# Optimization experiments

Measured on AMD Instinct MI355X. Metric: run time of the kernel, lower is better.

Reference implementation:

```python
import jax, jax.numpy as jnp
import numpy as np

N, D, S, H, QP, VP = 512, 256, 32, 4, 8, 8
PAIR_C = S + 3 * VP          # 56
P3 = H * QP * 3              # 96
FD = P3 + 16                 # 112 (rel + dist rbf)


def _layer_norm(x, scale, offset, eps=1e-5):
    mu = x.mean(-1, keepdims=True)
    var = ((x - mu) ** 2).mean(-1, keepdims=True)
    return (x - mu) * jax.lax.rsqrt(var + eps) * scale + offset


def _distance_rbf(d, bins=16, min_d=0.0, max_d=22.0):
    # Gaussian RBF featurization of pairwise distances (salad distance_rbf).
    step = (max_d - min_d) / bins
    centers = min_d + step * jnp.arange(bins, dtype=d.dtype) + step / 2
    return jnp.exp(-(((d[..., None] - centers) / step) ** 2))


def setup_inputs() -> dict:
    key = jax.random.key(0)
    ks = jax.random.split(key, 16)
    f32 = jnp.float32
    nrm = lambda k, shape, s=1.0: (s * jax.random.normal(k, shape)).astype(f32)
    HS = H * S
    return {
        "local": nrm(ks[0], (N, D)),
        "pos": nrm(ks[1], (N, 5, 3)),
        "resi": jnp.arange(N, dtype=jnp.int32),
        "chain": jax.random.randint(ks[2], (N,), 0, 2, dtype=jnp.int32),
        "batch": jnp.zeros((N,), dtype=jnp.int32),
        "mask": jnp.ones((N,), dtype=bool),
        "q_ln_scale": jnp.ones((S,), f32),
        "q_ln_offset": jnp.zeros((S,), f32),
        "k_ln_scale": jnp.ones((S,), f32),
        "k_ln_offset": jnp.zeros((S,), f32),
        "w_q": nrm(ks[3], (D, HS), D ** -0.5),
        "b_q": jnp.zeros((HS,), f32),
        "w_k": nrm(ks[4], (D, HS), D ** -0.5),
        "b_k": jnp.zeros((HS,), f32),
        "w_v": nrm(ks[5], (D, HS), D ** -0.5),
        "b_v": jnp.zeros((HS,), f32),
        "w_qp": nrm(ks[6], (D, H * QP * 3), 0.1 * D ** -0.5),
        "b_qp": jnp.zeros((H * QP * 3,), f32),
        "w_kp": nrm(ks[7], (D, H * QP * 3), 0.1 * D ** -0.5),
        "b_kp": jnp.zeros((H * QP * 3,), f32),
        "w_vp": nrm(ks[8], (D, H * VP * 3), 0.1 * D ** -0.5),
        "b_vp": jnp.zeros((H * VP * 3,), f32),
        "resi_embedding": nrm(ks[9], (66, PAIR_C), 66 ** -0.5),
        "w_pair": nrm(ks[10], (FD, PAIR_C), FD ** -0.5),
        "w_bias": nrm(ks[11], (FD, H), FD ** -0.5),
        "b_bias": jnp.zeros((H,), f32),
        "gamma": jnp.full((H,), np.log(np.e - 1.0), f32),
        "w_out": nrm(ks[12], (H * PAIR_C, D), (H * PAIR_C) ** -0.5),
    }


def reference(local, pos, resi, chain, batch, mask,
              q_ln_scale, q_ln_offset, k_ln_scale, k_ln_offset,
              w_q, b_q, w_k, b_k, w_v, b_v,
              w_qp, b_qp, w_kp, b_kp, w_vp, b_vp,
              resi_embedding, w_pair, w_bias, b_bias, gamma, w_out):
    n = local.shape[0]
    ca = pos[:, 1]  # [n,3]

    q = _layer_norm((local @ w_q + b_q).reshape(n, H, S), q_ln_scale, q_ln_offset)
    k = _layer_norm((local @ w_k + b_k).reshape(n, H, S), k_ln_scale, k_ln_offset)
    v = (local @ w_v + b_v).reshape(n, H, S)
    qp = (local @ w_qp + b_qp).reshape(n, H, QP, 3) + ca[:, None, None]
    kp = (local @ w_kp + b_kp).reshape(n, H, QP, 3) + ca[:, None, None]
    vp = (local @ w_vp + b_vp).reshape(n, H, VP, 3) + ca[:, None, None]
    value = jnp.concatenate((v, vp.reshape(n, H, 3 * VP)), axis=-1)  # [n,H,56]

    same_batch = batch[:, None] == batch[None, :]
    pair_mask = (mask[:, None] & mask[None, :]) & same_batch  # [n,n]

    inner = jnp.einsum('ihc,jhc->ijh', q * jnp.sqrt(1.0 / S), k)  # [n,n,H]
    diff = qp[:, None] - kp[None, :]                 # [n,n,H,QP,3]
    point_att = -(diff ** 2).sum(axis=(-1, -2))      # [n,n,H]
    rel = diff.reshape(n, n, P3)                     # [n,n,96]

    dca = 10.0 * ca
    dist = jnp.sqrt(((dca[:, None] - dca[None, :]) ** 2).sum(-1) + 1e-6)
    dist = _distance_rbf(dist)                       # [n,n,16]

    resi_dist = jnp.clip(resi[:, None] - resi[None, :], -32, 32)
    other_chain = chain[:, None] != chain[None, :]
    rdist = jnp.where(other_chain, 65, resi_dist + 32)
    emb = resi_embedding[rdist]                      # [n,n,56]

    feat = jnp.concatenate((rel, dist), axis=-1)     # [n,n,112]
    pair = emb + feat @ w_pair                       # [n,n,56]
    bias = feat @ w_bias + b_bias                    # [n,n,H]
    pair = pair[:, :, None, :] + value[None]         # [n,n,H,56]

    w_C = jnp.sqrt(2.0 / (9 * QP))
    point_scale = jax.nn.softplus(gamma).reshape(1, 1, H) * w_C / 2

    attn = (inner + point_scale * point_att + bias) * jnp.sqrt(1.0 / 3.0)
    attn = jnp.where(pair_mask[..., None], attn, -1e9)
    attn = jax.nn.softmax(attn, axis=1)
    attn = jnp.where(pair_mask[..., None], attn, 0.0)

    result = jnp.einsum('ijh,ijhc->ihc', attn, pair).reshape(n, -1)  # [n,224]
    return result @ w_out                             # [n,D]
```

## Files before the change

kernel.cpp:

```cpp
#include <hip/hip_runtime.h>
#include <hip/hip_bf16.h>
#include <cstddef>

#define N_NODES 512
#define DIM     256
#define H_HEADS 4
#define PAIR_CN 56
#define P3_N    96
#define FD_N    112
#define HPC     224

typedef _Float16 h2v  __attribute__((ext_vector_type(2)));
typedef _Float16 f16x8 __attribute__((ext_vector_type(8)));
typedef float    f32x4 __attribute__((ext_vector_type(4)));

__device__ __forceinline__ bool mask_true(const void* m, int idx) {
    if (((const unsigned char*)m)[idx] != 0) return true;
    return ((const int*)m)[idx] != 0;
}
__device__ __forceinline__ unsigned packh2(float a, float b) {
    _Float16 ha = (_Float16)a, hb = (_Float16)b;
    unsigned short ua, ub;
    __builtin_memcpy(&ua, &ha, 2); __builtin_memcpy(&ub, &hb, 2);
    return (unsigned)ua | ((unsigned)ub << 16);
}
__device__ __forceinline__ float h2lof(unsigned u) {
    unsigned short t = (unsigned short)(u & 0xffff);
    _Float16 h; __builtin_memcpy(&h, &t, 2); return (float)h;
}
__device__ __forceinline__ float h2hif(unsigned u) {
    unsigned short t = (unsigned short)(u >> 16);
    _Float16 h; __builtin_memcpy(&h, &t, 2); return (float)h;
}
__device__ __forceinline__ float dot2u(unsigned a, unsigned b, float c) {
#if __has_builtin(__builtin_amdgcn_fdot2)
    h2v ha, hb;
    __builtin_memcpy(&ha, &a, 4);
    __builtin_memcpy(&hb, &b, 4);
    return __builtin_amdgcn_fdot2(ha, hb, c, false);
#else
    return c + h2lof(a)*h2lof(b) + h2hif(a)*h2hif(b);
#endif
}
__device__ __forceinline__ f32x4 mfma16(uint4 a, uint4 b, f32x4 c) {
    f16x8 af, bf;
    __builtin_memcpy(&af, &a, 16);
    __builtin_memcpy(&bf, &b, 16);
    return __builtin_amdgcn_mfma_f32_16x16x32_f16(af, bf, c, 0, 0, 0);
}

__global__ __launch_bounds__(512) void proj_kernel(
    const float* __restrict__ local, const float* __restrict__ pos,
    const float* __restrict__ qls, const float* __restrict__ qlo,
    const float* __restrict__ kls, const float* __restrict__ klo,
    const float* __restrict__ w_q, const float* __restrict__ b_q,
    const float* __restrict__ w_k, const float* __restrict__ b_k,
    const float* __restrict__ w_v, const float* __restrict__ b_v,
    const float* __restrict__ w_qp, const float* __restrict__ b_qp,
    const float* __restrict__ w_kp, const float* __restrict__ b_kp,
    const float* __restrict__ w_vp, const float* __restrict__ b_vp,
    const float* __restrict__ w_bias, const float* __restrict__ b_bias,
    const float* __restrict__ gamma,
    const float* __restrict__ remb, const float* __restrict__ w_pair,
    const float* __restrict__ w_out,
    unsigned* __restrict__ qnP, unsigned* __restrict__ knT4,
    unsigned* __restrict__ qpP, unsigned* __restrict__ kpT4,
    unsigned* __restrict__ BF,
    unsigned* __restrict__ woPk, unsigned* __restrict__ wp2,
    unsigned* __restrict__ remb2,
    float* __restrict__ jinfo, float* __restrict__ iinfo)
{
    const int i0 = blockIdx.x * 2;
    const int tid = threadIdx.x;

    __shared__ float xL[2][DIM];
    __shared__ float qraw[2][128];
    __shared__ float kraw[2][128];
    __shared__ float stat[2][16];
    __shared__ float qpL[2][P3_N];
    __shared__ float kpbL[2][P3_N];
    __shared__ float wbS[384];

    if (blockIdx.x < 16) {
        for (int t = blockIdx.x*512 + tid; t < 33656; t += 8192) {
            if (t < 28672) {
                const int t2 = t >> 8, colx = t & 255;
                woPk[t] = packh2(w_out[(size_t)(2*t2)*DIM + colx],
                                 w_out[(size_t)(2*t2 + 1)*DIM + colx]);
            } else if (t < 31808) {
                const int v = t - 28672, f2 = v / 56, cx = v % 56;
                wp2[v] = packh2(w_pair[(2*f2)*PAIR_CN + cx],
                                w_pair[(2*f2 + 1)*PAIR_CN + cx]);
            } else {
                const int v = t - 31808, r2 = v / 56, cx = v % 56;
                remb2[v] = packh2(remb[(2*r2)*PAIR_CN + cx],
                                  remb[(2*r2 + 1)*PAIR_CN + cx]);
            }
        }
    }

    {
        const int r = tid >> 8, d = tid & 255;
        xL[r][d] = local[(size_t)(i0 + r) * DIM + d];
    }
    if (tid < 384) wbS[tid] = w_bias[tid];
    __syncthreads();

    const int cstBF = ((i0 >> 5) << 8) + (((i0 >> 3) & 3) << 6) + ((i0 >> 1) & 3);

    if (tid < 336) {
        const int colg = tid >> 1, dh = tid & 1;
        const int col = colg * 4;
        const float* w; int width, c, seg;
        if      (col < 128) { w = w_q;  c = col;       width = 128; seg = 0; }
        else if (col < 256) { w = w_k;  c = col - 128; width = 128; seg = 1; }
        else if (col < 384) { w = w_v;  c = col - 256; width = 128; seg = 2; }
        else if (col < 480) { w = w_qp; c = col - 384; width = 96;  seg = 3; }
        else if (col < 576) { w = w_kp; c = col - 480; width = 96;  seg = 4; }
        else                { w = w_vp; c = col - 576; width = 96;  seg = 5; }

        float acc[2][4] = {{0.f,0.f,0.f,0.f},{0.f,0.f,0.f,0.f}};
        const float* wc = w + c;
        const int dbase = dh * 128;
#pragma unroll 1
        for (int bb = 0; bb < 16; ++bb) {
            const int d0 = dbase + bb*8;
            const float4 wv0 = *(const float4*)(wc + (size_t)(d0 + 0)*width);
            const float4 wv1 = *(const float4*)(wc + (size_t)(d0 + 1)*width);
            const float4 wv2 = *(const float4*)(wc + (size_t)(d0 + 2)*width);
            const float4 wv3 = *(const float4*)(wc + (size_t)(d0 + 3)*width);
            const float4 wv4 = *(const float4*)(wc + (size_t)(d0 + 4)*width);
            const float4 wv5 = *(const float4*)(wc + (size_t)(d0 + 5)*width);
            const float4 wv6 = *(const float4*)(wc + (size_t)(d0 + 6)*width);
            const float4 wv7 = *(const float4*)(wc + (size_t)(d0 + 7)*width);
#pragma unroll
            for (int r = 0; r < 2; ++r) {
                const float x0 = xL[r][d0 + 0], x1 = xL[r][d0 + 1];
                const float x2 = xL[r][d0 + 2], x3 = xL[r][d0 + 3];
                const float x4 = xL[r][d0 + 4], x5 = xL[r][d0 + 5];
                const float x6 = xL[r][d0 + 6], x7 = xL[r][d0 + 7];
                acc[r][0] += x0*wv0.x + x1*wv1.x + x2*wv2.x + x3*wv3.x
                           + x4*wv4.x + x5*wv5.x + x6*wv6.x + x7*wv7.x;
                acc[r][1] += x0*wv0.y + x1*wv1.y + x2*wv2.y + x3*wv3.y
                           + x4*wv4.y + x5*wv5.y + x6*wv6.y + x7*wv7.y;
                acc[r][2] += x0*wv0.z + x1*wv1.z + x2*wv2.z + x3*wv3.z
                           + x4*wv4.z + x5*wv5.z + x6*wv6.z + x7*wv7.z;
                acc[r][3] += x0*wv0.w + x1*wv1.w + x2*wv2.w + x3*wv3.w
                           + x4*wv4.w + x5*wv5.w + x6*wv6.w + x7*wv7.w;
            }
        }
#pragma unroll
        for (int r = 0; r < 2; ++r)
#pragma unroll
            for (int e = 0; e < 4; ++e)
                acc[r][e] += __shfl_xor(acc[r][e], 1);

        if (dh == 0) {
            const float cax0 = pos[i0*15+3],     cay0 = pos[i0*15+4],     caz0 = pos[i0*15+5];
            const float cax1 = pos[(i0+1)*15+3], cay1 = pos[(i0+1)*15+4], caz1 = pos[(i0+1)*15+5];
            float fr0[4], fr1[4];
            const bool isKp = (seg == 4), isQp = (seg == 3);
#pragma unroll
            for (int e = 0; e < 4; ++e) {
                const int cc = c + e;
                const float v0 = acc[0][e], v1 = acc[1][e];
                if (seg == 0) {
                    qraw[0][cc] = v0 + b_q[cc];
                    qraw[1][cc] = v1 + b_q[cc];
                } else if (seg == 1) {
                    kraw[0][cc] = v0 + b_k[cc];
                    kraw[1][cc] = v1 + b_k[cc];
                } else if (seg == 2) {
                    const int h = cc >> 5, sc = cc & 31;
                    const int colF = h*PAIR_CN + sc;
                    BF[(colF >> 4)*4096 + (colF & 15)*4 + cstBF] =
                        packh2(v0 + b_v[cc], v1 + b_v[cc]);
                } else if (seg == 3) {
                    const int x = cc % 3;
                    const float cav0 = (x==0)?cax0:((x==1)?cay0:caz0);
                    const float cav1 = (x==0)?cax1:((x==1)?cay1:caz1);
                    const float r0 = v0 + b_qp[cc] + cav0;
                    const float r1 = v1 + b_qp[cc] + cav1;
                    fr0[e] = r0; fr1[e] = r1;
                    qpL[0][cc] = r0; qpL[1][cc] = r1;
                } else if (seg == 4) {
                    const int x = cc % 3;
                    const float cav0 = (x==0)?cax0:((x==1)?cay0:caz0);
                    const float cav1 = (x==0)?cax1:((x==1)?cay1:caz1);
                    const float r0 = v0 + b_kp[cc] + cav0;
                    const float r1 = v1 + b_kp[cc] + cav1;
                    fr0[e] = r0; fr1[e] = r1;
                    const int colF = 224 + cc;
                    BF[(colF >> 4)*4096 + (colF & 15)*4 + cstBF] = packh2(r0, r1);
                    kpbL[0][cc] = (float)(_Float16)r0;
                    kpbL[1][cc] = (float)(_Float16)r1;
                } else {
                    const int h = cc / 24, rr = cc % 24, x = cc % 3;
                    const float cav0 = (x==0)?cax0:((x==1)?cay0:caz0);
                    const float cav1 = (x==0)?cax1:((x==1)?cay1:caz1);
                    const int colF = h*PAIR_CN + 32 + rr;
                    BF[(colF >> 4)*4096 + (colF & 15)*4 + cstBF] =
                        packh2(v0 + b_vp[cc] + cav0, v1 + b_vp[cc] + cav1);
                }
            }
            if (isQp) {
                const int f2 = c >> 1;
                qpP[(size_t)i0*48 + f2]         = packh2(fr0[0], fr0[1]);
                qpP[(size_t)i0*48 + f2 + 1]     = packh2(fr0[2], fr0[3]);
                qpP[(size_t)(i0+1)*48 + f2]     = packh2(fr1[0], fr1[1]);
                qpP[(size_t)(i0+1)*48 + f2 + 1] = packh2(fr1[2], fr1[3]);
            }
            if (isKp) {
                const int f2 = c >> 1;
                const int fq = f2 >> 2;
                kpT4[((size_t)fq*N_NODES + i0    )*4 + (f2 & 3)]       = packh2(fr0[0], fr0[1]);
                kpT4[((size_t)fq*N_NODES + i0    )*4 + ((f2 + 1) & 3)] = packh2(fr0[2], fr0[3]);
                kpT4[((size_t)fq*N_NODES + i0 + 1)*4 + (f2 & 3)]       = packh2(fr1[0], fr1[1]);
                kpT4[((size_t)fq*N_NODES + i0 + 1)*4 + ((f2 + 1) & 3)] = packh2(fr1[2], fr1[3]);
            }
        }
    }
    __syncthreads();

    if (tid < 16) {
        const int r = tid >> 3, t = tid & 7;
        const float* src = (t < 4) ? qraw[r] : kraw[r];
        const int h = t & 3, base = (t < 4) ? 0 : 8;
        float mu = 0.f;
        for (int c = 0; c < 32; ++c) mu += src[h*32 + c];
        mu *= (1.f/32.f);
        float var = 0.f;
        for (int c = 0; c < 32; ++c) { float d = src[h*32 + c] - mu; var += d*d; }
        var *= (1.f/32.f);
        stat[r][base + h*2 + 0] = mu;
        stat[r][base + h*2 + 1] = var;
    }
    __syncthreads();

    {
        const int r = tid >> 8, u = tid & 255;
        const int i = i0 + r;
        if (u < 128) {
            const int h = u >> 5, sidx = u & 31;
            const float mu = stat[r][h*2], var = stat[r][h*2+1];
            float v = (qraw[r][u] - mu) * rsqrtf(var + 1e-5f) * qls[sidx] + qlo[sidx];
            v *= 0.17677669529663687f;
            const float vo = __shfl_xor(v, 1);
            if (!(u & 1)) qnP[(size_t)i*64 + (u >> 1)] = packh2(v, vo);
        } else {
            const int u2 = u - 128, h = u2 >> 5, sidx = u2 & 31;
            const float mu = stat[r][8 + h*2], var = stat[r][9 + h*2];
            float v = (kraw[r][u2] - mu) * rsqrtf(var + 1e-5f) * kls[sidx] + klo[sidx];
            const float vo = __shfl_xor(v, 1);
            if (!(u2 & 1))
                knT4[(((size_t)(u2 >> 3))*N_NODES + i)*4 + ((u2 >> 1) & 3)] = packh2(v, vo);
        }
    }

    if (tid < 64) {
        const int r = tid >> 5, h = (tid >> 3) & 3, ks = tid & 7;
        float uacc = 0.f, tacc = 0.f;
#pragma unroll
        for (int f = ks; f < P3_N; f += 8) {
            float wb = wbS[f*4 + h];
            uacc += qpL[r][f] * wb;
            tacc += kpbL[r][f] * wb;
        }
        float nq = 0.f, nk = 0.f;
#pragma unroll
        for (int f = h*24 + ks*3; f < h*24 + ks*3 + 3; ++f) {
            nq += qpL[r][f]*qpL[r][f];
            nk += kpbL[r][f]*kpbL[r][f];
        }
        uacc += __shfl_xor(uacc,1); uacc += __shfl_xor(uacc,2); uacc += __shfl_xor(uacc,4);
        tacc += __shfl_xor(tacc,1); tacc += __shfl_xor(tacc,2); tacc += __shfl_xor(tacc,4);
        nq   += __shfl_xor(nq,1);   nq   += __shfl_xor(nq,2);   nq   += __shfl_xor(nq,4);
        nk   += __shfl_xor(nk,1);   nk   += __shfl_xor(nk,2);   nk   += __shfl_xor(nk,4);
        if (ks == 0) {
            const int n = i0 + r;
            const float ps = log1pf(expf(gamma[h])) * (1.0f/12.0f);
            iinfo[n*4 + h] = -ps*nq + uacc + b_bias[h];
            jinfo[n*8 + h] = -ps*nk - tacc;
            if (h == 0) {
                jinfo[n*8 + 4] = 10.f * pos[n*15 + 3];
                jinfo[n*8 + 5] = 10.f * pos[n*15 + 4];
                jinfo[n*8 + 6] = 10.f * pos[n*15 + 5];
                jinfo[n*8 + 7] = 0.f;
            }
        }
    }
}

__global__ __launch_bounds__(1024, 4) void attn_kernel(
    const unsigned* __restrict__ qnP, const unsigned* __restrict__ knT4,
    const unsigned* __restrict__ qpP, const unsigned* __restrict__ kpT4,
    const unsigned* __restrict__ BF,
    const unsigned* __restrict__ woPk, const unsigned* __restrict__ wp2,
    const unsigned* __restrict__ remb2,
    const float* __restrict__ jinfo, const float* __restrict__ iinfo,
    const int* __restrict__ resi, const int* __restrict__ chain,
    const int* __restrict__ batch, const void* __restrict__ maskp,
    const float* __restrict__ w_bias, const float* __restrict__ gamma,
    float* __restrict__ out)
{
    const int ib   = blockIdx.x * 2;
    const int tid  = threadIdx.x;
    const int lane = tid & 63;
    const int wv   = tid >> 6;
    const int hp   = tid >> 9;
    const int j    = tid & 511;

    __shared__ unsigned qpkL[2][64];
    __shared__ unsigned qspkL[2][48];
    __shared__ unsigned wbPk[H_HEADS][8];
    __shared__ __align__(16) unsigned rbfP[2][N_NODES][9];
    __shared__ __align__(16) unsigned attnH2[8][260];
    __shared__ float    mxW[16][4], smW[16][4];
    __shared__ float    asL2[2][H_HEADS];
    __shared__ float    qpiL2[2][P3_N];
    __shared__ float    GLfF2[2][H_HEADS][P3_N];
    __shared__ float    GLfR2[2][H_HEADS][16];
    __shared__ unsigned GLf22[2][H_HEADS][56];
    __shared__ unsigned abktP2[2][H_HEADS][33];
    __shared__ float    resL2[2][HPC];
    __shared__ unsigned resH2[2][FD_N];
    __shared__ float    abktW8[8][2][H_HEADS][66];

    if (tid < 128) {
        const int r = tid >> 6, u = tid & 63;
        qpkL[r][u] = qnP[(size_t)(ib + r)*64 + u];
    } else if (tid < 224) {
        const int v = tid - 128, r = v / 48, f2 = v % 48;
        const int h = f2 / 12;
        const float ps2 = 2.f * log1pf(expf(gamma[h])) * (1.0f/12.0f);
        const unsigned u = qpP[(size_t)(ib + r)*48 + f2];
        qspkL[r][f2] = packh2(ps2*h2lof(u), ps2*h2hif(u));
    } else if (tid < 320) {
        const int v = tid - 224, r = v / 48, f2 = v % 48;
        const unsigned u = qpP[(size_t)(ib + r)*48 + f2];
        qpiL2[r][2*f2]   = h2lof(u);
        qpiL2[r][2*f2+1] = h2hif(u);
    } else if (tid < 352) {
        const int v = tid - 320, h = v >> 3, e = v & 7;
        wbPk[h][e] = packh2(w_bias[(P3_N + 2*e)*H_HEADS + h],
                            w_bias[(P3_N + 2*e + 1)*H_HEADS + h]);
    }
    for (int t = tid; t < 8*2*H_HEADS*66; t += 1024) ((float*)abktW8)[t] = 0.f;

    const int  ri0 = resi[ib], ri1 = resi[ib+1];
    const int  ch0 = chain[ib], ch1 = chain[ib+1];
    const int  ba0 = batch[ib], ba1 = batch[ib+1];
    const bool mi0 = mask_true(maskp, ib), mi1 = mask_true(maskp, ib+1);
    const float dix0 = jinfo[(size_t)ib*8+4], diy0 = jinfo[(size_t)ib*8+5], diz0 = jinfo[(size_t)ib*8+6];
    const float dix1 = jinfo[(size_t)(ib+1)*8+4], diy1 = jinfo[(size_t)(ib+1)*8+5], diz1 = jinfo[(size_t)(ib+1)*8+6];

    const float inv3  = 0.57735026918962576f;
    const float rstep = 0.72727272727272727f;

    const float4 vq4 = *(const float4*)(jinfo + (size_t)j*8);
    const float4 dj4 = *(const float4*)(jinfo + (size_t)j*8 + 4);
    const float4 ciA = *(const float4*)(iinfo + (size_t)ib*4);
    const float4 ciB = *(const float4*)(iinfo + (size_t)(ib+1)*4);
    const float vqa[4] = {vq4.x, vq4.y, vq4.z, vq4.w};
    const float cia[2][4] = {{ciA.x, ciA.y, ciA.z, ciA.w},
                             {ciB.x, ciB.y, ciB.z, ciB.w}};
    {
        const float dx = (hp ? dix1 : dix0) - dj4.x;
        const float dy = (hp ? diy1 : diy0) - dj4.y;
        const float dz = (hp ? diz1 : diz0) - dj4.z;
        const float dist = sqrtf(dx*dx + dy*dy + dz*dz + 1e-6f);
#pragma unroll
        for (int p = 0; p < 8; ++p) {
            const float u0 = (dist - (1.375f*(float)(2*p)   + 0.6875f)) * rstep;
            const float u1 = (dist - (1.375f*(float)(2*p+1) + 0.6875f)) * rstep;
            rbfP[hp][j][p] = packh2(__expf(-u0*u0), __expf(-u1*u1));
        }
    }
    const int  rj = resi[j], cj = chain[j], bj = batch[j];
    const bool mj = mask_true(maskp, j);
    bool pmv[2];
    int  rdv[2];
    pmv[0] = mi0 && mj && (ba0 == bj);
    pmv[1] = mi1 && mj && (ba1 == bj);
    rdv[0] = (ch0 != cj) ? 65 : (min(max(ri0 - rj, -32), 32) + 32);
    rdv[1] = (ch1 != cj) ? 65 : (min(max(ri1 - rj, -32), 32) + 32);
    __syncthreads();

    float lv[2][2];
    {
        const int h0 = hp*2, h1 = hp*2 + 1;
        const uint4* kcol = (const uint4*)knT4 + j;
        const uint4* pcol = (const uint4*)kpT4 + j;
        const uint4 ka0 = kcol[(size_t)(h0*4 + 0)*N_NODES];
        const uint4 ka1 = kcol[(size_t)(h0*4 + 1)*N_NODES];
        const uint4 ka2 = kcol[(size_t)(h0*4 + 2)*N_NODES];
        const uint4 ka3 = kcol[(size_t)(h0*4 + 3)*N_NODES];
        const uint4 kb0 = kcol[(size_t)(h1*4 + 0)*N_NODES];
        const uint4 kb1 = kcol[(size_t)(h1*4 + 1)*N_NODES];
        const uint4 kb2 = kcol[(size_t)(h1*4 + 2)*N_NODES];
        const uint4 kb3 = kcol[(size_t)(h1*4 + 3)*N_NODES];
        const uint4 pa0 = pcol[(size_t)(h0*3 + 0)*N_NODES];
        const uint4 pa1 = pcol[(size_t)(h0*3 + 1)*N_NODES];
        const uint4 pa2 = pcol[(size_t)(h0*3 + 2)*N_NODES];
        const uint4 pb0 = pcol[(size_t)(h1*3 + 0)*N_NODES];
        const uint4 pb1 = pcol[(size_t)(h1*3 + 1)*N_NODES];
        const uint4 pb2 = pcol[(size_t)(h1*3 + 2)*N_NODES];
        const uint4 rr0a = *(const uint4*)&rbfP[0][j][0];
        const uint4 rr0b = *(const uint4*)&rbfP[0][j][4];
        const uint4 rr1a = *(const uint4*)&rbfP[1][j][0];
        const uint4 rr1b = *(const uint4*)&rbfP[1][j][4];
        const uint4 w0a = *(const uint4*)&wbPk[h0][0];
        const uint4 w0b = *(const uint4*)&wbPk[h0][4];
        const uint4 w1a = *(const uint4*)&wbPk[h1][0];
        const uint4 w1b = *(const uint4*)&wbPk[h1][4];
#pragma unroll
        for (int r = 0; r < 2; ++r) {
            const uint4* qk4 = (const uint4*)&qpkL[r][0];
            const uint4* qs4 = (const uint4*)&qspkL[r][0];
            const uint4 rra = r ? rr1a : rr0a;
            const uint4 rrb = r ? rr1b : rr0b;
            float a0 = 0.f;
            {
                const uint4 q0 = qk4[h0*4 + 0], q1 = qk4[h0*4 + 1];
                const uint4 q2 = qk4[h0*4 + 2], q3 = qk4[h0*4 + 3];
                a0 = dot2u(ka0.x, q0.x, a0); a0 = dot2u(ka0.y, q0.y, a0);
                a0 = dot2u(ka0.z, q0.z, a0); a0 = dot2u(ka0.w, q0.w, a0);
                a0 = dot2u(ka1.x, q1.x, a0); a0 = dot2u(ka1.y, q1.y, a0);
                a0 = dot2u(ka1.z, q1.z, a0); a0 = dot2u(ka1.w, q1.w, a0);
                a0 = dot2u(ka2.x, q2.x, a0); a0 = dot2u(ka2.y, q2.y, a0);
                a0 = dot2u(ka2.z, q2.z, a0); a0 = dot2u(ka2.w, q2.w, a0);
                a0 = dot2u(ka3.x, q3.x, a0); a0 = dot2u(ka3.y, q3.y, a0);
                a0 = dot2u(ka3.z, q3.z, a0); a0 = dot2u(ka3.w, q3.w, a0);
                const uint4 s0 = qs4[h0*3 + 0], s1 = qs4[h0*3 + 1], s2 = qs4[h0*3 + 2];
                a0 = dot2u(pa0.x, s0.x, a0); a0 = dot2u(pa0.y, s0.y, a0);
                a0 = dot2u(pa0.z, s0.z, a0); a0 = dot2u(pa0.w, s0.w, a0);
                a0 = dot2u(pa1.x, s1.x, a0); a0 = dot2u(pa1.y, s1.y, a0);
                a0 = dot2u(pa1.z, s1.z, a0); a0 = dot2u(pa1.w, s1.w, a0);
                a0 = dot2u(pa2.x, s2.x, a0); a0 = dot2u(pa2.y, s2.y, a0);
                a0 = dot2u(pa2.z, s2.z, a0); a0 = dot2u(pa2.w, s2.w, a0);
                a0 = dot2u(rra.x, w0a.x, a0); a0 = dot2u(rra.y, w0a.y, a0);
                a0 = dot2u(rra.z, w0a.z, a0); a0 = dot2u(rra.w, w0a.w, a0);
                a0 = dot2u(rrb.x, w0b.x, a0); a0 = dot2u(rrb.y, w0b.y, a0);
                a0 = dot2u(rrb.z, w0b.z, a0); a0 = dot2u(rrb.w, w0b.w, a0);
            }
            lv[r][0] = pmv[r] ? (a0 + cia[r][h0] + vqa[h0]) * inv3 : -1e9f;
            float a1 = 0.f;
            {
                const uint4 q0 = qk4[h1*4 + 0], q1 = qk4[h1*4 + 1];
                const uint4 q2 = qk4[h1*4 + 2], q3 = qk4[h1*4 + 3];
                a1 = dot2u(kb0.x, q0.x, a1); a1 = dot2u(kb0.y, q0.y, a1);
                a1 = dot2u(kb0.z, q0.z, a1); a1 = dot2u(kb0.w, q0.w, a1);
                a1 = dot2u(kb1.x, q1.x, a1); a1 = dot2u(kb1.y, q1.y, a1);
                a1 = dot2u(kb1.z, q1.z, a1); a1 = dot2u(kb1.w, q1.w, a1);
                a1 = dot2u(kb2.x, q2.x, a1); a1 = dot2u(kb2.y, q2.y, a1);
                a1 = dot2u(kb2.z, q2.z, a1); a1 = dot2u(kb2.w, q2.w, a1);
                a1 = dot2u(kb3.x, q3.x, a1); a1 = dot2u(kb3.y, q3.y, a1);
                a1 = dot2u(kb3.z, q3.z, a1); a1 = dot2u(kb3.w, q3.w, a1);
                const uint4 s0 = qs4[h1*3 + 0], s1 = qs4[h1*3 + 1], s2 = qs4[h1*3 + 2];
                a1 = dot2u(pb0.x, s0.x, a1); a1 = dot2u(pb0.y, s0.y, a1);
                a1 = dot2u(pb0.z, s0.z, a1); a1 = dot2u(pb0.w, s0.w, a1);
                a1 = dot2u(pb1.x, s1.x, a1); a1 = dot2u(pb1.y, s1.y, a1);
                a1 = dot2u(pb1.z, s1.z, a1); a1 = dot2u(pb1.w, s1.w, a1);
                a1 = dot2u(pb2.x, s2.x, a1); a1 = dot2u(pb2.y, s2.y, a1);
                a1 = dot2u(pb2.z, s2.z, a1); a1 = dot2u(pb2.w, s2.w, a1);
                a1 = dot2u(rra.x, w1a.x, a1); a1 = dot2u(rra.y, w1a.y, a1);
                a1 = dot2u(rra.z, w1a.z, a1); a1 = dot2u(rra.w, w1a.w, a1);
                a1 = dot2u(rrb.x, w1b.x, a1); a1 = dot2u(rrb.y, w1b.y, a1);
                a1 = dot2u(rrb.z, w1b.z, a1); a1 = dot2u(rrb.w, w1b.w, a1);
            }
            lv[r][1] = pmv[r] ? (a1 + cia[r][h1] + vqa[h1]) * inv3 : -1e9f;
        }
    }

    {
        float mx[4] = {lv[0][0], lv[0][1], lv[1][0], lv[1][1]};
#pragma unroll
        for (int off = 1; off < 64; off <<= 1) {
#pragma unroll
            for (int s = 0; s < 4; ++s) mx[s] = fmaxf(mx[s], __shfl_xor(mx[s], off));
        }
        if (lane == 0) *(float4*)&mxW[wv][0] = make_float4(mx[0], mx[1], mx[2], mx[3]);
        __syncthreads();
        float mxg[4] = {-1e30f, -1e30f, -1e30f, -1e30f};
        const int wbase = hp*8;
#pragma unroll
        for (int w = 0; w < 8; ++w) {
            const float4 m = *(const float4*)&mxW[wbase + w][0];
            mxg[0] = fmaxf(mxg[0], m.x); mxg[1] = fmaxf(mxg[1], m.y);
            mxg[2] = fmaxf(mxg[2], m.z); mxg[3] = fmaxf(mxg[3], m.w);
        }
        float e[4], sm[4];
        e[0] = pmv[0] ? __expf(lv[0][0] - mxg[0]) : 0.f;
        e[1] = pmv[0] ? __expf(lv[0][1] - mxg[1]) : 0.f;
        e[2] = pmv[1] ? __expf(lv[1][0] - mxg[2]) : 0.f;
        e[3] = pmv[1] ? __expf(lv[1][1] - mxg[3]) : 0.f;
#pragma unroll
        for (int s = 0; s < 4; ++s) sm[s] = e[s];
#pragma unroll
        for (int off = 1; off < 64; off <<= 1) {
#pragma unroll
            for (int s = 0; s < 4; ++s) sm[s] += __shfl_xor(sm[s], off);
        }
        if (lane == 0) *(float4*)&smW[wv][0] = make_float4(sm[0], sm[1], sm[2], sm[3]);
        __syncthreads();
        float smt[4] = {0.f, 0.f, 0.f, 0.f};
#pragma unroll
        for (int w = 0; w < 8; ++w) {
            const float4 m = *(const float4*)&smW[wbase + w][0];
            smt[0] += m.x; smt[1] += m.y; smt[2] += m.z; smt[3] += m.w;
        }
        float p[4];
#pragma unroll
        for (int s = 0; s < 4; ++s) {
            const float rden = 1.f / fmaxf(smt[s], 1e-37f);
            p[s] = e[s] * rden;
        }
        const int h0 = hp*2;
        atomicAdd(&abktW8[wv & 7][0][h0    ][rdv[0]], p[0]);
        atomicAdd(&abktW8[wv & 7][0][h0 + 1][rdv[0]], p[1]);
        atomicAdd(&abktW8[wv & 7][1][h0    ][rdv[1]], p[2]);
        atomicAdd(&abktW8[wv & 7][1][h0 + 1][rdv[1]], p[3]);
        if (j == 0) {
            asL2[0][h0]     = smt[0] / fmaxf(smt[0], 1e-37f);
            asL2[0][h0 + 1] = smt[1] / fmaxf(smt[1], 1e-37f);
            asL2[1][h0]     = smt[2] / fmaxf(smt[2], 1e-37f);
            asL2[1][h0 + 1] = smt[3] / fmaxf(smt[3], 1e-37f);
        }
#pragma unroll
        for (int s = 0; s < 4; ++s) {
            const float po = __shfl_xor(p[s], 1);
            if (!(j & 1)) {
                const int r = s >> 1, hh = s & 1;
                attnH2[r*4 + h0 + hh][j >> 1] = packh2(p[s], po);
            }
        }
    }
    __syncthreads();

    if (wv < 14) {
        const int row = lane & 15;
        const int ntA = wv;
        const int ntB = (wv < 6) ? (wv + 14) : -1;
        f32x4 accA = {0.f,0.f,0.f,0.f};
        f32x4 accB = {0.f,0.f,0.f,0.f};
        const uint4* bfp = (const uint4*)BF;
#pragma unroll 4
        for (int kt = 0; kt < 16; ++kt) {
            uint4 au = make_uint4(0u, 0u, 0u, 0u);
            if (row < 8) au = *(const uint4*)&attnH2[row][kt*16 + (lane >> 4)*4];
            const uint4 bA = bfp[(ntA*16 + kt)*64 + lane];
            accA = mfma16(au, bA, accA);
            if (ntB >= 0) {
                const uint4 bB = bfp[(ntB*16 + kt)*64 + lane];
                accB = mfma16(au, bB, accB);
            }
        }
        if (lane < 32) {
            const int r = lane >> 4, c16 = lane & 15;
            {
                const int s = ntA*16 + c16;
                if (s < HPC) {
                    resL2[r][s] = ((const float*)&accA)[s / PAIR_CN];
                } else {
                    const int f = s - HPC;
                    GLfF2[r][0][f] = accA[0];
                    GLfF2[r][1][f] = accA[1];
                    GLfF2[r][2][f] = accA[2];
                    GLfF2[r][3][f] = accA[3];
                }
            }
            if (ntB >= 0) {
                const int s = ntB*16 + c16;
                if (s < HPC) {
                    resL2[r][s] = ((const float*)&accB)[s / PAIR_CN];
                } else {
                    const int f = s - HPC;
                    GLfF2[r][0][f] = accB[0];
                    GLfF2[r][1][f] = accB[1];
                    GLfF2[r][2][f] = accB[2];
                    GLfF2[r][3][f] = accB[3];
                }
            }
        }
    } else {
        const int r = wv - 14;
        const int b = lane >> 2, q = lane & 3;
        const int w = b >> 1;
        const bool hi = (b & 1);
        float a[4] = {0.f, 0.f, 0.f, 0.f};
#pragma unroll 4
        for (int jpp = q*64; jpp < q*64 + 64; ++jpp) {
            const unsigned r0 = rbfP[r][2*jpp][w];
            const unsigned r1 = rbfP[r][2*jpp + 1][w];
            const unsigned ee = hi ? ((r0 >> 16) | (r1 & 0xffff0000u))
                                   : ((r0 & 0xffffu) | (r1 << 16));
            a[0] = dot2u(ee, attnH2[r*4 + 0][jpp], a[0]);
            a[1] = dot2u(ee, attnH2[r*4 + 1][jpp], a[1]);
            a[2] = dot2u(ee, attnH2[r*4 + 2][jpp], a[2]);
            a[3] = dot2u(ee, attnH2[r*4 + 3][jpp], a[3]);
        }
#pragma unroll
        for (int h = 0; h < 4; ++h) {
            a[h] += __shfl_xor(a[h], 1);
            a[h] += __shfl_xor(a[h], 2);
            if (q == 0) GLfR2[r][h][b] = a[h];
        }
    }
    __syncthreads();

    for (int t = tid; t < 448; t += 1024) {
        const int r = t / 224, v = t % 224, h = v / 56, f2 = v % 56;
        if (f2 < 48) {
            GLf22[r][h][f2] = packh2(qpiL2[r][2*f2]*asL2[r][h]     - GLfF2[r][h][2*f2],
                                     qpiL2[r][2*f2 + 1]*asL2[r][h] - GLfF2[r][h][2*f2 + 1]);
        } else {
            GLf22[r][h][f2] = packh2(GLfR2[r][h][(f2 - 48)*2], GLfR2[r][h][(f2 - 48)*2 + 1]);
        }
    }
    for (int t = tid; t < 264; t += 1024) {
        const int r = t / 132, v = t % 132, h = v / 33, r2 = v % 33;
        float s0 = 0.f, s1 = 0.f;
#pragma unroll
        for (int w = 0; w < 8; ++w) {
            s0 += abktW8[w][r][h][2*r2];
            s1 += abktW8[w][r][h][2*r2 + 1];
        }
        abktP2[r][h][r2] = packh2(s0, s1);
    }
    __syncthreads();

    if (tid < HPC) {
        const int h = tid / PAIR_CN, c = tid - h*PAIR_CN;
        float r0 = resL2[0][tid];
        float r1 = resL2[1][tid];
        {
            unsigned buf[16];
#pragma unroll
            for (int t = 0; t < 16; ++t) buf[t] = remb2[t*56 + c];
#pragma unroll
            for (int t = 0; t < 16; ++t) {
                r0 = dot2u(buf[t], abktP2[0][h][t], r0);
                r1 = dot2u(buf[t], abktP2[1][h][t], r1);
            }
#pragma unroll
            for (int t = 0; t < 16; ++t) buf[t] = remb2[(16 + t)*56 + c];
#pragma unroll
            for (int t = 0; t < 16; ++t) {
                r0 = dot2u(buf[t], abktP2[0][h][16 + t], r0);
                r1 = dot2u(buf[t], abktP2[1][h][16 + t], r1);
            }
            const unsigned b32 = remb2[32*56 + c];
            r0 = dot2u(b32, abktP2[0][h][32], r0);
            r1 = dot2u(b32, abktP2[1][h][32], r1);
        }
        {
            unsigned buf[14];
#pragma unroll
            for (int qq = 0; qq < 4; ++qq) {
#pragma unroll
                for (int t = 0; t < 14; ++t) buf[t] = wp2[(qq*14 + t)*56 + c];
#pragma unroll
                for (int t = 0; t < 14; ++t) {
                    r0 = dot2u(buf[t], GLf22[0][h][qq*14 + t], r0);
                    r1 = dot2u(buf[t], GLf22[1][h][qq*14 + t], r1);
                }
            }
        }
        resL2[0][tid] = r0;
        resL2[1][tid] = r1;
    }
    __syncthreads();

    if (tid < 2*FD_N) {
        const int r = tid / FD_N, t2 = tid % FD_N;
        resH2[r][t2] = packh2(resL2[r][2*t2], resL2[r][2*t2 + 1]);
    }
    __syncthreads();

    if (tid < 512) {
        const int col = tid >> 1, ph = tid & 1;
        float o0 = 0.f, o1 = 0.f;
        unsigned buf[14];
#pragma unroll
        for (int qq = 0; qq < 4; ++qq) {
            const int base = ph*56 + qq*14;
#pragma unroll
            for (int t = 0; t < 14; ++t) buf[t] = woPk[(base + t)*256 + col];
#pragma unroll
            for (int t = 0; t < 14; ++t) {
                o0 = dot2u(buf[t], resH2[0][base + t], o0);
                o1 = dot2u(buf[t], resH2[1][base + t], o1);
            }
        }
        o0 += __shfl_xor(o0, 1);
        o1 += __shfl_xor(o1, 1);
        if (ph == 0) {
            out[(size_t)ib*DIM + col]       = o0;
            out[(size_t)(ib + 1)*DIM + col] = o1;
        }
    }
}

extern "C" void kernel_launch(void* const* d_in, const int* in_sizes, int n_in,
                              void* d_out, int out_size, void* d_ws, size_t ws_size,
                              hipStream_t stream) {
    (void)in_sizes; (void)n_in; (void)out_size; (void)ws_size;
    const float* local = (const float*)d_in[0];
    const float* pos   = (const float*)d_in[1];
    const int*   resi  = (const int*)d_in[2];
    const int*   chain = (const int*)d_in[3];
    const int*   batch = (const int*)d_in[4];
    const void*  maskp = d_in[5];
    const float* qls   = (const float*)d_in[6];
    const float* qlo   = (const float*)d_in[7];
    const float* kls   = (const float*)d_in[8];
    const float* klo   = (const float*)d_in[9];
    const float* w_q   = (const float*)d_in[10];
    const float* b_q   = (const float*)d_in[11];
    const float* w_k   = (const float*)d_in[12];
    const float* b_k   = (const float*)d_in[13];
    const float* w_v   = (const float*)d_in[14];
    const float* b_v   = (const float*)d_in[15];
    const float* w_qp  = (const float*)d_in[16];
    const float* b_qp  = (const float*)d_in[17];
    const float* w_kp  = (const float*)d_in[18];
    const float* b_kp  = (const float*)d_in[19];
    const float* w_vp  = (const float*)d_in[20];
    const float* b_vp  = (const float*)d_in[21];
    const float* remb  = (const float*)d_in[22];
    const float* w_pair= (const float*)d_in[23];
    const float* w_bias= (const float*)d_in[24];
    const float* b_bias= (const float*)d_in[25];
    const float* gamma = (const float*)d_in[26];
    const float* w_out = (const float*)d_in[27];

    char* ws = (char*)d_ws;
    unsigned* qnP   = (unsigned*)(ws);
    unsigned* qpP   = (unsigned*)(ws + 131072);
    unsigned* knT4  = (unsigned*)(ws + 229376);
    unsigned* kpT4  = (unsigned*)(ws + 360448);
    unsigned* BF    = (unsigned*)(ws + 458752);
    float*    jinf  = (float*)(ws + 786432);
    float*    iinf  = (float*)(ws + 802816);
    unsigned* woPk  = (unsigned*)(ws + 811008);
    unsigned* wp2   = (unsigned*)(ws + 925696);
    unsigned* remb2 = (unsigned*)(ws + 938240);

    proj_kernel<<<N_NODES / 2, 512, 0, stream>>>(
        local, pos, qls, qlo, kls, klo,
        w_q, b_q, w_k, b_k, w_v, b_v,
        w_qp, b_qp, w_kp, b_kp, w_vp, b_vp,
        w_bias, b_bias, gamma,
        remb, w_pair, w_out,
        qnP, knT4, qpP, kpT4, BF,
        woPk, wp2, remb2, jinf, iinf);

    attn_kernel<<<N_NODES / 2, 1024, 0, stream>>>(
        qnP, knT4, qpP, kpT4, BF,
        woPk, wp2, remb2, jinf, iinf,
        resi, chain, batch, maskp,
        w_bias, gamma,
        (float*)d_out);
}
```

Measured before the change: 53.62 us.

## Fuse projection and attention kernels with a software grid barrier

Merges the projection kernel and the attention kernel into one persistent launch of 1024-thread blocks. A global atomic-counter barrier, reset with a memset before each launch, separates the two phases. The projection reduction over the feature dimension is split four ways instead of two, with an extra shuffle to combine the partial sums. The aim is to remove the second kernel launch and the gap between kernels. The risks are a deadlock if the 256 blocks cannot all be resident at once, the cost of the spin barrier, and lower occupancy from the larger combined shared-memory footprint.

```diff
diff --git a/kernel.cpp b/kernel.cpp
--- a/kernel.cpp
+++ b/kernel.cpp
@@ -49,7 +49,7 @@
     return __builtin_amdgcn_mfma_f32_16x16x32_f16(af, bf, c, 0, 0, 0);
 }
 
-__global__ __launch_bounds__(512) void proj_kernel(
+__global__ __launch_bounds__(1024) void fused_kernel(
     const float* __restrict__ local, const float* __restrict__ pos,
     const float* __restrict__ qls, const float* __restrict__ qlo,
     const float* __restrict__ kls, const float* __restrict__ klo,
@@ -63,14 +63,19 @@
     const float* __restrict__ gamma,
     const float* __restrict__ remb, const float* __restrict__ w_pair,
     const float* __restrict__ w_out,
+    const int* __restrict__ resi, const int* __restrict__ chain,
+    const int* __restrict__ batch, const void* __restrict__ maskp,
     unsigned* __restrict__ qnP, unsigned* __restrict__ knT4,
     unsigned* __restrict__ qpP, unsigned* __restrict__ kpT4,
     unsigned* __restrict__ BF,
     unsigned* __restrict__ woPk, unsigned* __restrict__ wp2,
     unsigned* __restrict__ remb2,
-    float* __restrict__ jinfo, float* __restrict__ iinfo)
+    float* __restrict__ jinfo, float* __restrict__ iinfo,
+    unsigned* __restrict__ barCnt,
+    float* __restrict__ out)
 {
-    const int i0 = blockIdx.x * 2;
+    const int ib  = blockIdx.x * 2;
+    const int i0  = ib;
     const int tid = threadIdx.x;
 
     __shared__ float xL[2][DIM];
@@ -80,9 +85,24 @@
     __shared__ float qpL[2][P3_N];
     __shared__ float kpbL[2][P3_N];
     __shared__ float wbS[384];
+    __shared__ unsigned qpkL[2][64];
+    __shared__ unsigned qspkL[2][48];
+    __shared__ unsigned wbPk[H_HEADS][8];
+    __shared__ __align__(16) unsigned rbfP[2][N_NODES][9];
+    __shared__ __align__(16) unsigned attnH2[8][260];
+    __shared__ float    mxW[16][4], smW[16][4];
+    __shared__ float    asL2[2][H_HEADS];
+    __shared__ float    qpiL2[2][P3_N];
+    __shared__ float    GLfF2[2][H_HEADS][P3_N];
+    __shared__ float    GLfR2[2][H_HEADS][16];
+    __shared__ unsigned GLf22[2][H_HEADS][56];
+    __shared__ unsigned abktP2[2][H_HEADS][33];
+    __shared__ float    resL2[2][HPC];
+    __shared__ unsigned resH2[2][FD_N];
+    __shared__ float    abktW8[8][2][H_HEADS][66];
 
     if (blockIdx.x < 16) {
-        for (int t = blockIdx.x*512 + tid; t < 33656; t += 8192) {
+        for (int t = blockIdx.x*1024 + tid; t < 33656; t += 16384) {
             if (t < 28672) {
                 const int t2 = t >> 8, colx = t & 255;
                 woPk[t] = packh2(w_out[(size_t)(2*t2)*DIM + colx],
@@ -99,17 +119,17 @@
         }
     }
 
-    {
+    if (tid < 512) {
         const int r = tid >> 8, d = tid & 255;
         xL[r][d] = local[(size_t)(i0 + r) * DIM + d];
     }
-    if (tid < 384) wbS[tid] = w_bias[tid];
+    if (tid >= 512 && tid < 896) wbS[tid - 512] = w_bias[tid - 512];
     __syncthreads();
 
     const int cstBF = ((i0 >> 5) << 8) + (((i0 >> 3) & 3) << 6) + ((i0 >> 1) & 3);
 
-    if (tid < 336) {
-        const int colg = tid >> 1, dh = tid & 1;
+    if (tid < 672) {
+        const int colg = tid >> 2, dq = tid & 3;
         const int col = colg * 4;
         const float* w; int width, c, seg;
         if      (col < 128) { w = w_q;  c = col;       width = 128; seg = 0; }
@@ -121,9 +141,9 @@
 
         float acc[2][4] = {{0.f,0.f,0.f,0.f},{0.f,0.f,0.f,0.f}};
         const float* wc = w + c;
-        const int dbase = dh * 128;
+        const int dbase = dq * 64;
 #pragma unroll 1
-        for (int bb = 0; bb < 16; ++bb) {
+        for (int bb = 0; bb < 8; ++bb) {
             const int d0 = dbase + bb*8;
             const float4 wv0 = *(const float4*)(wc + (size_t)(d0 + 0)*width);
             const float4 wv1 = *(const float4*)(wc + (size_t)(d0 + 1)*width);
@@ -152,10 +172,12 @@
 #pragma unroll
         for (int r = 0; r < 2; ++r)
 #pragma unroll
-            for (int e = 0; e < 4; ++e)
+            for (int e = 0; e < 4; ++e) {
                 acc[r][e] += __shfl_xor(acc[r][e], 1);
-
-        if (dh == 0) {
+                acc[r][e] += __shfl_xor(acc[r][e], 2);
+            }
+
+        if (dq == 0) {
             const float cax0 = pos[i0*15+3],     cay0 = pos[i0*15+4],     caz0 = pos[i0*15+5];
             const float cax1 = pos[(i0+1)*15+3], cay1 = pos[(i0+1)*15+4], caz1 = pos[(i0+1)*15+5];
             float fr0[4], fr1[4];
@@ -237,7 +259,7 @@
     }
     __syncthreads();
 
-    {
+    if (tid < 512) {
         const int r = tid >> 8, u = tid & 255;
         const int i = i0 + r;
         if (u < 128) {
@@ -289,42 +311,23 @@
             }
         }
     }
-}
-
-__global__ __launch_bounds__(1024, 4) void attn_kernel(
-    const unsigned* __restrict__ qnP, const unsigned* __restrict__ knT4,
-    const unsigned* __restrict__ qpP, const unsigned* __restrict__ kpT4,
-    const unsigned* __restrict__ BF,
-    const unsigned* __restrict__ woPk, const unsigned* __restrict__ wp2,
-    const unsigned* __restrict__ remb2,
-    const float* __restrict__ jinfo, const float* __restrict__ iinfo,
-    const int* __restrict__ resi, const int* __restrict__ chain,
-    const int* __restrict__ batch, const void* __restrict__ maskp,
-    const float* __restrict__ w_bias, const float* __restrict__ gamma,
-    float* __restrict__ out)
-{
-    const int ib   = blockIdx.x * 2;
-    const int tid  = threadIdx.x;
+
+    __threadfence();
+    __syncthreads();
+    if (tid == 0) {
+        atomicAdd(barCnt, 1u);
+        while (__hip_atomic_load(barCnt, __ATOMIC_ACQUIRE,
+                                 __HIP_MEMORY_SCOPE_AGENT) < (unsigned)gridDim.x) {
+            __builtin_amdgcn_s_sleep(1);
+        }
+    }
+    __syncthreads();
+    __threadfence();
+
     const int lane = tid & 63;
     const int wv   = tid >> 6;
     const int hp   = tid >> 9;
     const int j    = tid & 511;
-
-    __shared__ unsigned qpkL[2][64];
-    __shared__ unsigned qspkL[2][48];
-    __shared__ unsigned wbPk[H_HEADS][8];
-    __shared__ __align__(16) unsigned rbfP[2][N_NODES][9];
-    __shared__ __align__(16) unsigned attnH2[8][260];
-    __shared__ float    mxW[16][4], smW[16][4];
-    __shared__ float    asL2[2][H_HEADS];
-    __shared__ float    qpiL2[2][P3_N];
-    __shared__ float    GLfF2[2][H_HEADS][P3_N];
-    __shared__ float    GLfR2[2][H_HEADS][16];
-    __shared__ unsigned GLf22[2][H_HEADS][56];
-    __shared__ unsigned abktP2[2][H_HEADS][33];
-    __shared__ float    resL2[2][HPC];
-    __shared__ unsigned resH2[2][FD_N];
-    __shared__ float    abktW8[8][2][H_HEADS][66];
 
     if (tid < 128) {
         const int r = tid >> 6, u = tid & 63;
@@ -409,10 +412,10 @@
         const uint4 rr0b = *(const uint4*)&rbfP[0][j][4];
         const uint4 rr1a = *(const uint4*)&rbfP[1][j][0];
         const uint4 rr1b = *(const uint4*)&rbfP[1][j][4];
-        const uint4 w0a = *(const uint4*)&wbPk[h0][0];
-        const uint4 w0b = *(const uint4*)&wbPk[h0][4];
-        const uint4 w1a = *(const uint4*)&wbPk[h1][0];
-        const uint4 w1b = *(const uint4*)&wbPk[h1][4];
+        const uint4 w0a = *(const uint4*)&wbPk[hp*2][0];
+        const uint4 w0b = *(const uint4*)&wbPk[hp*2][4];
+        const uint4 w1a = *(const uint4*)&wbPk[hp*2 + 1][0];
+        const uint4 w1b = *(const uint4*)&wbPk[hp*2 + 1][4];
 #pragma unroll
         for (int r = 0; r < 2; ++r) {
             const uint4* qk4 = (const uint4*)&qpkL[r][0];
@@ -745,20 +748,19 @@
     unsigned* woPk  = (unsigned*)(ws + 811008);
     unsigned* wp2   = (unsigned*)(ws + 925696);
     unsigned* remb2 = (unsigned*)(ws + 938240);
-
-    proj_kernel<<<N_NODES / 2, 512, 0, stream>>>(
+    unsigned* barC  = (unsigned*)(ws + 945664);
+
+    hipMemsetAsync(barC, 0, 4, stream);
+
+    fused_kernel<<<N_NODES / 2, 1024, 0, stream>>>(
         local, pos, qls, qlo, kls, klo,
         w_q, b_q, w_k, b_k, w_v, b_v,
         w_qp, b_qp, w_kp, b_kp, w_vp, b_vp,
         w_bias, b_bias, gamma,
         remb, w_pair, w_out,
-        qnP, knT4, qpP, kpT4, BF,
-        woPk, wp2, remb2, jinf, iinf);
-
-    attn_kernel<<<N_NODES / 2, 1024, 0, stream>>>(
+        resi, chain, batch, maskp,
         qnP, knT4, qpP, kpT4, BF,
         woPk, wp2, remb2, jinf, iinf,
-        resi, chain, batch, maskp,
-        w_bias, gamma,
+        barC,
         (float*)d_out);
 }
```

Result: slower. 201.4 us (+275.7%).
